# Optimization experiments

Measured on AMD Instinct MI355X. Metric: run time of the kernel, lower is better.

Reference implementation:

```python
import jax, jax.numpy as jnp
import numpy as np

N_NODES = 50000
N_EDGES = 800000


def setup_inputs() -> dict:
    key = jax.random.key(0)
    ks = jax.random.split(key, 9)
    d, h, hd = 128, 4, 32
    s = 1.0 / np.sqrt(d)
    return {
        "x": jax.random.normal(ks[0], (N_NODES, d), jnp.float32),
        "edge_index": jax.random.randint(ks[1], (2, N_EDGES), 0, N_NODES, jnp.int32),
        "W0": jax.random.normal(ks[2], (d, d), jnp.float32) * s,
        "att_l0": jax.random.normal(ks[3], (h, hd), jnp.float32) * s,
        "att_r0": jax.random.normal(ks[4], (h, hd), jnp.float32) * s,
        "b0": jnp.zeros((d,), jnp.float32),
        "W1": jax.random.normal(ks[5], (d, d), jnp.float32) * s,
        "att_l1": jax.random.normal(ks[6], (h, hd), jnp.float32) * s,
        "att_r1": jax.random.normal(ks[7], (h, hd), jnp.float32) * s,
        "b1": jnp.zeros((hd,), jnp.float32),
    }


def _gat_layer(x, src, dst, W, att_l, att_r, bias, concat):
    # x: [N, F_in]; W: [H*D, F_in] (torch Linear layout); att_*: [H, D]
    n = x.shape[0]
    h, d = att_l.shape
    hx = (x @ W.T).reshape(n, h, d)                     # [N,H,D]
    al = jnp.einsum('nhd,hd->nh', hx, att_l)            # [N,H]
    ar = jnp.einsum('nhd,hd->nh', hx, att_r)
    att = al[src] + ar[dst]                             # [E,H]
    att = jax.nn.leaky_relu(att, negative_slope=0.2)
    # segment softmax over destination nodes
    m = jax.ops.segment_max(att, dst, num_segments=n)   # [N,H]
    att = jnp.exp(att - m[dst])
    ssum = jax.ops.segment_sum(att, dst, num_segments=n)
    att = att / (ssum[dst] + 1e-9)                      # [E,H]
    msgs = att[:, :, None] * hx[src]                    # [E,H,D]
    out = jax.ops.segment_sum(msgs, dst, num_segments=n)  # [N,H,D]
    if concat:
        out = out.reshape(n, h * d)
    else:
        out = out.mean(axis=1)
    return out + bias


def reference(x, edge_index, W0, att_l0, att_r0, b0, W1, att_l1, att_r1, b1):
    src, dst = edge_index[0], edge_index[1]
    x = _gat_layer(x, src, dst, W0, att_l0, att_r0, b0, concat=True)
    x = jax.nn.relu(x)  # dropout is identity in eval mode
    x = _gat_layer(x, src, dst, W1, att_l1, att_r1, b1, concat=False)
    return x
```

## Files before the change

kernel.cpp:

```cpp
#include <hip/hip_runtime.h>
#include <hip/hip_bf16.h>

#define H 4
#define D 32
#define F 128
#define MAXDEG 64
#define PF 16
#define NBUCK 256
#define BUCKW 196
#define CAP   4096
#define NABLK 128

typedef __attribute__((ext_vector_type(8))) short bf16x8;
typedef __attribute__((ext_vector_type(4))) float f32x4;

__device__ __forceinline__ short f2bf(float v) {
    __hip_bfloat16 h = __float2bfloat16(v);
    return *reinterpret_cast<short*>(&h);
}
__device__ __forceinline__ float bf2f(short s) {
    __hip_bfloat16 h = *reinterpret_cast<__hip_bfloat16*>(&s);
    return __bfloat162float(h);
}

__device__ __forceinline__
void wconv_body(const float* __restrict__ W, short* __restrict__ Whi,
                short* __restrict__ Wlo) {
    for (int i = threadIdx.x * 4; i < F * F; i += 1024) {
        float4 v = *reinterpret_cast<const float4*>(W + i);
        float vv[4] = {v.x, v.y, v.z, v.w};
        short hs[4], ls[4];
#pragma unroll
        for (int j = 0; j < 4; ++j) {
            hs[j] = f2bf(vv[j]);
            ls[j] = f2bf(vv[j] - bf2f(hs[j]));
        }
        *reinterpret_cast<short4*>(Whi + i) = make_short4(hs[0], hs[1], hs[2], hs[3]);
        *reinterpret_cast<short4*>(Wlo + i) = make_short4(ls[0], ls[1], ls[2], ls[3]);
    }
}

__device__ __forceinline__
void bucketA_body(int abid, const int* __restrict__ ei, int E,
                  int* __restrict__ gcnt, unsigned int* __restrict__ buf) {
    __shared__ int lcnt[NBUCK];
    __shared__ int lpos[NBUCK];
    const int tid = threadIdx.x;
    lcnt[tid] = 0;
    __syncthreads();
    const int per = ((E / NABLK) + 3) & ~3;
    const int e0 = abid * per;
    const int e1 = min(e0 + per, E);
    for (int e = e0 + 4 * tid; e < e1; e += 1024) {
        int4 dv = *reinterpret_cast<const int4*>(ei + E + e);
        atomicAdd(&lcnt[dv.x / BUCKW], 1);
        atomicAdd(&lcnt[dv.y / BUCKW], 1);
        atomicAdd(&lcnt[dv.z / BUCKW], 1);
        atomicAdd(&lcnt[dv.w / BUCKW], 1);
    }
    __syncthreads();
    if (lcnt[tid] > 0)
        lpos[tid] = atomicAdd(&gcnt[tid], lcnt[tid]);
    __syncthreads();
    for (int e = e0 + 4 * tid; e < e1; e += 1024) {
        int4 sv = *reinterpret_cast<const int4*>(ei + e);
        int4 dv = *reinterpret_cast<const int4*>(ei + E + e);
        int ss[4] = {sv.x, sv.y, sv.z, sv.w};
        int dd[4] = {dv.x, dv.y, dv.z, dv.w};
#pragma unroll
        for (int j = 0; j < 4; ++j) {
            int b = dd[j] / BUCKW;
            int pos = atomicAdd(&lpos[b], 1);
            if (pos < CAP)
                buf[(size_t)b * CAP + pos] =
                    (unsigned)ss[j] | ((unsigned)(dd[j] - b * BUCKW) << 16);
        }
    }
}

__global__ __launch_bounds__(256)
void k_prep(const float* __restrict__ W0, short* __restrict__ W0hi,
            short* __restrict__ W0lo, const float* __restrict__ W1,
            short* __restrict__ W1hi, short* __restrict__ W1lo,
            const int* __restrict__ ei, int E,
            int* __restrict__ gcnt, unsigned int* __restrict__ buf) {
    if (blockIdx.x < NABLK)
        bucketA_body(blockIdx.x, ei, E, gcnt, buf);
    else if (blockIdx.x == NABLK)
        wconv_body(W0, W0hi, W0lo);
    else
        wconv_body(W1, W1hi, W1lo);
}

__device__ __forceinline__
void bucketB_body(int b, const unsigned int* __restrict__ buf,
                  const int* __restrict__ gcnt, int* __restrict__ deg,
                  unsigned short* __restrict__ ssrc2u, int N) {
    __shared__ int cnt[BUCKW];
    const int tid = threadIdx.x;
    if (tid < BUCKW) cnt[tid] = 0;
    __syncthreads();
    const int mm = min(gcnt[b], CAP);
    const int m4 = mm & ~3;
    for (int i = 4 * tid; i < m4; i += 1024) {
        uint4 r = *reinterpret_cast<const uint4*>(buf + (size_t)b * CAP + i);
        unsigned rr[4] = {r.x, r.y, r.z, r.w};
#pragma unroll
        for (int j = 0; j < 4; ++j) {
            int src  = rr[j] & 0xffff;
            int ldst = rr[j] >> 16;
            int slot = atomicAdd(&cnt[ldst], 1);
            if (slot < MAXDEG)
                ssrc2u[(size_t)(b * BUCKW + ldst) * MAXDEG + slot] = (unsigned short)src;
        }
    }
    for (int i = m4 + tid; i < mm; i += 256) {
        unsigned rec = buf[(size_t)b * CAP + i];
        int src  = rec & 0xffff;
        int ldst = rec >> 16;
        int slot = atomicAdd(&cnt[ldst], 1);
        if (slot < MAXDEG)
            ssrc2u[(size_t)(b * BUCKW + ldst) * MAXDEG + slot] = (unsigned short)src;
    }
    __syncthreads();
    if (tid < BUCKW) {
        int node = b * BUCKW + tid;
        if (node < N) deg[node] = cnt[tid];
    }
}

template<bool AFP32>
__device__ __forceinline__
void gemm_core(int bid, int nblocks, const void* __restrict__ Xv,
               const short* __restrict__ Xlo_, const short* __restrict__ Whi,
               const short* __restrict__ Wlo, const float* __restrict__ attl,
               const float* __restrict__ attr, __hip_bfloat16* __restrict__ HXB,
               float* __restrict__ AL, float* __restrict__ AR, int ntiles) {
    const int wave = threadIdx.x >> 6;
    const int lane = threadIdx.x & 63;
    const int m    = lane & 15;
    const int q    = lane >> 4;
    const int q8   = q * 8;

    bf16x8 Bhi[2][4], Blo[2][4];
#pragma unroll
    for (int j = 0; j < 2; ++j) {
        const int fout = wave * 32 + j * 16 + m;
#pragma unroll
        for (int kc = 0; kc < 4; ++kc) {
            Bhi[j][kc] = *reinterpret_cast<const bf16x8*>(Whi + (size_t)fout * F + kc * 32 + q8);
            Blo[j][kc] = *reinterpret_cast<const bf16x8*>(Wlo + (size_t)fout * F + kc * 32 + q8);
        }
    }
    const float alw0  = attl[wave * 32 + m];
    const float alw16 = attl[wave * 32 + 16 + m];
    const float arw0  = attr[wave * 32 + m];
    const float arw16 = attr[wave * 32 + 16 + m];

    for (int tile = bid; tile < ntiles; tile += nblocks) {
        const int node0 = tile * 16;
        bf16x8 Ahi[4], Alo[4];
        if constexpr (AFP32) {
            const float* xp = reinterpret_cast<const float*>(Xv) + (size_t)(node0 + m) * F + q8;
#pragma unroll
            for (int kc = 0; kc < 4; ++kc) {
                float4 x0 = *reinterpret_cast<const float4*>(xp + kc * 32);
                float4 x1 = *reinterpret_cast<const float4*>(xp + kc * 32 + 4);
                float xv[8] = {x0.x, x0.y, x0.z, x0.w, x1.x, x1.y, x1.z, x1.w};
#pragma unroll
                for (int t = 0; t < 8; ++t) {
                    short h = f2bf(xv[t]);
                    Ahi[kc][t] = h;
                    Alo[kc][t] = f2bf(xv[t] - bf2f(h));
                }
            }
        } else {
            const short* xh = reinterpret_cast<const short*>(Xv) + (size_t)(node0 + m) * F + q8;
            const short* xl = Xlo_ + (size_t)(node0 + m) * F + q8;
#pragma unroll
            for (int kc = 0; kc < 4; ++kc) {
                Ahi[kc] = *reinterpret_cast<const bf16x8*>(xh + kc * 32);
                Alo[kc] = *reinterpret_cast<const bf16x8*>(xl + kc * 32);
            }
        }
        f32x4 acc0 = {0.f, 0.f, 0.f, 0.f};
        f32x4 acc1 = {0.f, 0.f, 0.f, 0.f};
#pragma unroll
        for (int kc = 0; kc < 4; ++kc) {
            acc0 = __builtin_amdgcn_mfma_f32_16x16x32_bf16(Ahi[kc], Bhi[0][kc], acc0, 0, 0, 0);
            acc1 = __builtin_amdgcn_mfma_f32_16x16x32_bf16(Ahi[kc], Bhi[1][kc], acc1, 0, 0, 0);
            acc0 = __builtin_amdgcn_mfma_f32_16x16x32_bf16(Ahi[kc], Blo[0][kc], acc0, 0, 0, 0);
            acc1 = __builtin_amdgcn_mfma_f32_16x16x32_bf16(Ahi[kc], Blo[1][kc], acc1, 0, 0, 0);
            acc0 = __builtin_amdgcn_mfma_f32_16x16x32_bf16(Alo[kc], Bhi[0][kc], acc0, 0, 0, 0);
            acc1 = __builtin_amdgcn_mfma_f32_16x16x32_bf16(Alo[kc], Bhi[1][kc], acc1, 0, 0, 0);
        }
        const int row0 = node0 + q * 4;
        const int col0 = wave * 32 + m;
#pragma unroll
        for (int r = 0; r < 4; ++r) {
            HXB[(size_t)(row0 + r) * F + col0]      = __float2bfloat16(acc0[r]);
            HXB[(size_t)(row0 + r) * F + col0 + 16] = __float2bfloat16(acc1[r]);
            float pal = acc0[r] * alw0 + acc1[r] * alw16;
            float par = acc0[r] * arw0 + acc1[r] * arw16;
#pragma unroll
            for (int o = 1; o < 16; o <<= 1) {
                pal += __shfl_xor(pal, o);
                par += __shfl_xor(par, o);
            }
            if (m == 0) {
                AL[(size_t)(row0 + r) * H + wave] = pal;
                AR[(size_t)(row0 + r) * H + wave] = par;
            }
        }
    }
}

__global__ __launch_bounds__(256)
void k_g0(const unsigned int* __restrict__ buf, const int* __restrict__ gcnt,
          int* __restrict__ deg, unsigned short* __restrict__ ssrc2u, int N,
          const float* __restrict__ X, const short* __restrict__ W0hi,
          const short* __restrict__ W0lo, const float* __restrict__ attl0,
          const float* __restrict__ attr0, __hip_bfloat16* __restrict__ HXB,
          float* __restrict__ AL, float* __restrict__ AR, int ntiles) {
    if (blockIdx.x < NBUCK)
        bucketB_body(blockIdx.x, buf, gcnt, deg, ssrc2u, N);
    else
        gemm_core<true>(blockIdx.x - NBUCK, gridDim.x - NBUCK, X, nullptr,
                        W0hi, W0lo, attl0, attr0, HXB, AL, AR, ntiles);
}

__global__ __launch_bounds__(256)
void k_gemm1(const short* __restrict__ X1hi, const short* __restrict__ X1lo,
             const short* __restrict__ W1hi, const short* __restrict__ W1lo,
             const float* __restrict__ attl, const float* __restrict__ attr,
             __hip_bfloat16* __restrict__ HXB, float* __restrict__ AL,
             float* __restrict__ AR, int ntiles) {
    gemm_core<false>(blockIdx.x, gridDim.x, X1hi, X1lo, W1hi, W1lo,
                     attl, attr, HXB, AL, AR, ntiles);
}

__device__ __forceinline__
int stage_node(int g, int t, int n, const unsigned short* __restrict__ ssrc2u,
               const int* __restrict__ deg, const float* __restrict__ AL,
               const float4 ar4, int (*sidx)[MAXDEG], float (*sw)[MAXDEG][H]) {
    const int cnt  = min(deg[n], MAXDEG);
    const int rcnt = (cnt + PF - 1) & ~(PF - 1);
    if (t < rcnt) {
        if (t < cnt) {
            int s = ssrc2u[n * MAXDEG + t];
            sidx[g][t] = s;
            float4 al4 = *reinterpret_cast<const float4*>(AL + (size_t)s * H);
            float a0 = al4.x + ar4.x; a0 = a0 > 0.f ? a0 : 0.2f * a0;
            float a1 = al4.y + ar4.y; a1 = a1 > 0.f ? a1 : 0.2f * a1;
            float a2 = al4.z + ar4.z; a2 = a2 > 0.f ? a2 : 0.2f * a2;
            float a3 = al4.w + ar4.w; a3 = a3 > 0.f ? a3 : 0.2f * a3;
            sw[g][t][0] = __expf(a0);
            sw[g][t][1] = __expf(a1);
            sw[g][t][2] = __expf(a2);
            sw[g][t][3] = __expf(a3);
        } else {
            sidx[g][t] = 0;
            sw[g][t][0] = 0.f; sw[g][t][1] = 0.f; sw[g][t][2] = 0.f; sw[g][t][3] = 0.f;
        }
    }
    __builtin_amdgcn_wave_barrier();
    return rcnt;
}

__device__ __forceinline__
void gather_node(int g, int t, int h, int rcnt, const __hip_bfloat16* __restrict__ HXB,
                 const int (*sidx)[MAXDEG], const float (*sw)[MAXDEG][H],
                 float& accx, float& accy, float& wsum) {
    for (int base = 0; base < rcnt; base += PF) {
        __hip_bfloat162 v[PF];
#pragma unroll
        for (int j = 0; j < PF; ++j) {
            int s = sidx[g][base + j];
            v[j] = *reinterpret_cast<const __hip_bfloat162*>(HXB + (size_t)s * F + 2 * t);
        }
#pragma unroll
        for (int j = 0; j < PF; ++j) {
            float w = sw[g][base + j][h];
            float2 f = __bfloat1622float2(v[j]);
            accx += w * f.x;
            accy += w * f.y;
            wsum += w;
        }
    }
}

__global__ __launch_bounds__(256)
void k_aggr0(const unsigned short* __restrict__ ssrc2u, const int* __restrict__ deg,
             const float* __restrict__ AL, const float* __restrict__ AR,
             const __hip_bfloat16* __restrict__ HXB, const float* __restrict__ bias,
             short* __restrict__ X1hi, short* __restrict__ X1lo, int N) {
    __shared__ int   sidx[4][MAXDEG];
    __shared__ float sw[4][MAXDEG][H];
    const int g = threadIdx.x >> 6;
    const int t = threadIdx.x & 63;
    const int n = blockIdx.x * 4 + g;
    if (n >= N) return;
    const int h = t >> 4;
    const float4 ar4 = *reinterpret_cast<const float4*>(AR + (size_t)n * H);
    int rcnt = stage_node(g, t, n, ssrc2u, deg, AL, ar4, sidx, sw);
    float accx = 0.f, accy = 0.f, wsum = 0.f;
    gather_node(g, t, h, rcnt, HXB, sidx, sw, accx, accy, wsum);
    float inv = 1.f / (wsum + 1e-9f);
    float ox = fmaxf(accx * inv + bias[2 * t], 0.f);
    float oy = fmaxf(accy * inv + bias[2 * t + 1], 0.f);
    short h0 = f2bf(ox), h1 = f2bf(oy);
    short l0 = f2bf(ox - bf2f(h0)), l1 = f2bf(oy - bf2f(h1));
    unsigned hw = (unsigned)(unsigned short)h0 | ((unsigned)(unsigned short)h1 << 16);
    unsigned lw = (unsigned)(unsigned short)l0 | ((unsigned)(unsigned short)l1 << 16);
    *reinterpret_cast<unsigned*>(X1hi + (size_t)n * F + 2 * t) = hw;
    *reinterpret_cast<unsigned*>(X1lo + (size_t)n * F + 2 * t) = lw;
}

__global__ __launch_bounds__(256)
void k_aggr1(const unsigned short* __restrict__ ssrc2u, const int* __restrict__ deg,
             const float* __restrict__ AL, const float* __restrict__ AR,
             const __hip_bfloat16* __restrict__ HXB, const float* __restrict__ bias,
             float* __restrict__ out, int N) {
    __shared__ int   sidx[4][MAXDEG];
    __shared__ float sw[4][MAXDEG][H];
    const int g = threadIdx.x >> 6;
    const int t = threadIdx.x & 63;
    const int n = blockIdx.x * 4 + g;
    if (n >= N) return;
    const int h = t >> 4;
    const float4 ar4 = *reinterpret_cast<const float4*>(AR + (size_t)n * H);
    int rcnt = stage_node(g, t, n, ssrc2u, deg, AL, ar4, sidx, sw);
    float accx = 0.f, accy = 0.f, wsum = 0.f;
    gather_node(g, t, h, rcnt, HXB, sidx, sw, accx, accy, wsum);
    float inv = 1.f / (wsum + 1e-9f);
    float vx = accx * inv, vy = accy * inv;
    vx += __shfl_xor(vx, 16); vx += __shfl_xor(vx, 32);
    vy += __shfl_xor(vy, 16); vy += __shfl_xor(vy, 32);
    if (t < 16) {
        float2 o;
        o.x = 0.25f * vx + bias[2 * t];
        o.y = 0.25f * vy + bias[2 * t + 1];
        *reinterpret_cast<float2*>(out + (size_t)n * D + 2 * t) = o;
    }
}

extern "C" void kernel_launch(void* const* d_in, const int* in_sizes, int n_in,
                              void* d_out, int out_size, void* d_ws, size_t ws_size,
                              hipStream_t stream) {
    const float* x     = (const float*)d_in[0];
    const int*   ei    = (const int*)d_in[1];
    const float* W0    = (const float*)d_in[2];
    const float* attl0 = (const float*)d_in[3];
    const float* attr0 = (const float*)d_in[4];
    const float* b0    = (const float*)d_in[5];
    const float* W1    = (const float*)d_in[6];
    const float* attl1 = (const float*)d_in[7];
    const float* attr1 = (const float*)d_in[8];
    const float* b1    = (const float*)d_in[9];

    const int N = in_sizes[0] / F;
    const int E = in_sizes[1] / 2;
    const int ntiles = N / 16;

    char* p = (char*)d_ws;
    __hip_bfloat16* HXB = (__hip_bfloat16*)p;   p += (size_t)N * F * 2;
    short* X1hi = (short*)p;                    p += (size_t)N * F * 2;
    short* X1lo = (short*)p;                    p += (size_t)N * F * 2;
    short* W0hi = (short*)p;                    p += (size_t)F * F * 2;
    short* W0lo = (short*)p;                    p += (size_t)F * F * 2;
    short* W1hi = (short*)p;                    p += (size_t)F * F * 2;
    short* W1lo = (short*)p;                    p += (size_t)F * F * 2;
    float* AL   = (float*)p;                    p += (size_t)N * H * 4;
    float* AR   = (float*)p;                    p += (size_t)N * H * 4;
    unsigned short* ssrc2u = (unsigned short*)p; p += (size_t)N * MAXDEG * 2;
    int* deg = (int*)p;                         p += (size_t)N * 4;
    unsigned int* buf = (unsigned int*)p;       p += (size_t)NBUCK * CAP * 4;
    int* gcnt = (int*)p;

    hipMemsetAsync(gcnt, 0, NBUCK * sizeof(int), stream);

    k_prep<<<NABLK + 2, 256, 0, stream>>>(W0, W0hi, W0lo, W1, W1hi, W1lo,
                                          ei, E, gcnt, buf);

    k_g0<<<NBUCK + ntiles, 256, 0, stream>>>(buf, gcnt, deg, ssrc2u, N,
                                             x, W0hi, W0lo, attl0, attr0,
                                             HXB, AL, AR, ntiles);

    k_aggr0<<<(N + 3) / 4, 256, 0, stream>>>(ssrc2u, deg, AL, AR, HXB, b0,
                                             X1hi, X1lo, N);

    k_gemm1<<<ntiles, 256, 0, stream>>>(X1hi, X1lo, W1hi, W1lo, attl1, attr1,
                                        HXB, AL, AR, ntiles);

    k_aggr1<<<(N + 3) / 4, 256, 0, stream>>>(ssrc2u, deg, AL, AR, HXB, b1,
                                             (float*)d_out, N);
}
```

Before: 244.0 us.

## Fuse all GAT stages into one persistent cooperative kernel with grid syncs

Replaces the five launches (prep, bucketB+gemm0, aggr0, gemm1, aggr1) with one cooperative persistent kernel. Stages are separated by grid.sync, the layer-0 GEMM takes tiles from a dynamic atomic counter, and the W0 hi/lo split is done in registers instead of a separate conversion pass. The aim is to remove launch gaps and overlap bucketing with the first GEMM. In exchange, grid-wide barriers are costly, the grid is capped by occupancy, and the persistent loops may balance work worse than many small blocks did.

```diff
diff --git a/kernel.cpp b/kernel.cpp
--- a/kernel.cpp
+++ b/kernel.cpp
@@ -1,5 +1,8 @@
 #include <hip/hip_runtime.h>
 #include <hip/hip_bf16.h>
+#include <hip/hip_cooperative_groups.h>
+
+namespace cg = cooperative_groups;
 
 #define H 4
 #define D 32
@@ -9,7 +12,7 @@
 #define NBUCK 256
 #define BUCKW 196
 #define CAP   4096
-#define NABLK 128
+#define NABLK 256
 
 typedef __attribute__((ext_vector_type(8))) short bf16x8;
 typedef __attribute__((ext_vector_type(4))) float f32x4;
@@ -78,20 +81,6 @@
     }
 }
 
-__global__ __launch_bounds__(256)
-void k_prep(const float* __restrict__ W0, short* __restrict__ W0hi,
-            short* __restrict__ W0lo, const float* __restrict__ W1,
-            short* __restrict__ W1hi, short* __restrict__ W1lo,
-            const int* __restrict__ ei, int E,
-            int* __restrict__ gcnt, unsigned int* __restrict__ buf) {
-    if (blockIdx.x < NABLK)
-        bucketA_body(blockIdx.x, ei, E, gcnt, buf);
-    else if (blockIdx.x == NABLK)
-        wconv_body(W0, W0hi, W0lo);
-    else
-        wconv_body(W1, W1hi, W1lo);
-}
-
 __device__ __forceinline__
 void bucketB_body(int b, const unsigned int* __restrict__ buf,
                   const int* __restrict__ gcnt, int* __restrict__ deg,
@@ -129,20 +118,31 @@
     }
 }
 
-template<bool AFP32>
-__device__ __forceinline__
-void gemm_core(int bid, int nblocks, const void* __restrict__ Xv,
-               const short* __restrict__ Xlo_, const short* __restrict__ Whi,
-               const short* __restrict__ Wlo, const float* __restrict__ attl,
-               const float* __restrict__ attr, __hip_bfloat16* __restrict__ HXB,
-               float* __restrict__ AL, float* __restrict__ AR, int ntiles) {
-    const int wave = threadIdx.x >> 6;
-    const int lane = threadIdx.x & 63;
-    const int m    = lane & 15;
-    const int q    = lane >> 4;
-    const int q8   = q * 8;
-
-    bf16x8 Bhi[2][4], Blo[2][4];
+__device__ __forceinline__
+void bsetup_fp32(const float* __restrict__ W, int wave, int m, int q8,
+                 bf16x8 Bhi[2][4], bf16x8 Blo[2][4]) {
+#pragma unroll
+    for (int j = 0; j < 2; ++j) {
+        const int fout = wave * 32 + j * 16 + m;
+#pragma unroll
+        for (int kc = 0; kc < 4; ++kc) {
+            const float* wp = W + (size_t)fout * F + kc * 32 + q8;
+            float4 w0 = *reinterpret_cast<const float4*>(wp);
+            float4 w1 = *reinterpret_cast<const float4*>(wp + 4);
+            float wv[8] = {w0.x, w0.y, w0.z, w0.w, w1.x, w1.y, w1.z, w1.w};
+#pragma unroll
+            for (int t2 = 0; t2 < 8; ++t2) {
+                short hh = f2bf(wv[t2]);
+                Bhi[j][kc][t2] = hh;
+                Blo[j][kc][t2] = f2bf(wv[t2] - bf2f(hh));
+            }
+        }
+    }
+}
+
+__device__ __forceinline__
+void bsetup_pre(const short* __restrict__ Whi, const short* __restrict__ Wlo,
+                int wave, int m, int q8, bf16x8 Bhi[2][4], bf16x8 Blo[2][4]) {
 #pragma unroll
     for (int j = 0; j < 2; ++j) {
         const int fout = wave * 32 + j * 16 + m;
@@ -152,97 +152,86 @@
             Blo[j][kc] = *reinterpret_cast<const bf16x8*>(Wlo + (size_t)fout * F + kc * 32 + q8);
         }
     }
-    const float alw0  = attl[wave * 32 + m];
-    const float alw16 = attl[wave * 32 + 16 + m];
-    const float arw0  = attr[wave * 32 + m];
-    const float arw16 = attr[wave * 32 + 16 + m];
-
-    for (int tile = bid; tile < ntiles; tile += nblocks) {
-        const int node0 = tile * 16;
-        bf16x8 Ahi[4], Alo[4];
-        if constexpr (AFP32) {
-            const float* xp = reinterpret_cast<const float*>(Xv) + (size_t)(node0 + m) * F + q8;
-#pragma unroll
-            for (int kc = 0; kc < 4; ++kc) {
-                float4 x0 = *reinterpret_cast<const float4*>(xp + kc * 32);
-                float4 x1 = *reinterpret_cast<const float4*>(xp + kc * 32 + 4);
-                float xv[8] = {x0.x, x0.y, x0.z, x0.w, x1.x, x1.y, x1.z, x1.w};
-#pragma unroll
-                for (int t = 0; t < 8; ++t) {
-                    short h = f2bf(xv[t]);
-                    Ahi[kc][t] = h;
-                    Alo[kc][t] = f2bf(xv[t] - bf2f(h));
-                }
+}
+
+template<bool AFP32>
+__device__ __forceinline__
+void gemm_tile(int tile, const void* __restrict__ Xv, const short* __restrict__ Xlo_,
+               const bf16x8 Bhi[2][4], const bf16x8 Blo[2][4],
+               float alw0, float alw16, float arw0, float arw16,
+               __hip_bfloat16* __restrict__ HXB, float* __restrict__ AL,
+               float* __restrict__ AR, int wave, int m, int q) {
+    const int q8 = q * 8;
+    const int node0 = tile * 16;
+    bf16x8 Ahi[4], Alo[4];
+    if constexpr (AFP32) {
+        const float* xp = reinterpret_cast<const float*>(Xv) + (size_t)(node0 + m) * F + q8;
+#pragma unroll
+        for (int kc = 0; kc < 4; ++kc) {
+            float4 x0 = *reinterpret_cast<const float4*>(xp + kc * 32);
+            float4 x1 = *reinterpret_cast<const float4*>(xp + kc * 32 + 4);
+            float xv[8] = {x0.x, x0.y, x0.z, x0.w, x1.x, x1.y, x1.z, x1.w};
+#pragma unroll
+            for (int t2 = 0; t2 < 8; ++t2) {
+                short hh = f2bf(xv[t2]);
+                Ahi[kc][t2] = hh;
+                Alo[kc][t2] = f2bf(xv[t2] - bf2f(hh));
             }
-        } else {
-            const short* xh = reinterpret_cast<const short*>(Xv) + (size_t)(node0 + m) * F + q8;
-            const short* xl = Xlo_ + (size_t)(node0 + m) * F + q8;
-#pragma unroll
-            for (int kc = 0; kc < 4; ++kc) {
-                Ahi[kc] = *reinterpret_cast<const bf16x8*>(xh + kc * 32);
-                Alo[kc] = *reinterpret_cast<const bf16x8*>(xl + kc * 32);
-            }
-        }
-        f32x4 acc0 = {0.f, 0.f, 0.f, 0.f};
-        f32x4 acc1 = {0.f, 0.f, 0.f, 0.f};
+        }
+    } else {
+        const short* xh = reinterpret_cast<const short*>(Xv) + (size_t)(node0 + m) * F + q8;
+        const short* xl = Xlo_ + (size_t)(node0 + m) * F + q8;
 #pragma unroll
         for (int kc = 0; kc < 4; ++kc) {
-            acc0 = __builtin_amdgcn_mfma_f32_16x16x32_bf16(Ahi[kc], Bhi[0][kc], acc0, 0, 0, 0);
-            acc1 = __builtin_amdgcn_mfma_f32_16x16x32_bf16(Ahi[kc], Bhi[1][kc], acc1, 0, 0, 0);
-            acc0 = __builtin_amdgcn_mfma_f32_16x16x32_bf16(Ahi[kc], Blo[0][kc], acc0, 0, 0, 0);
-            acc1 = __builtin_amdgcn_mfma_f32_16x16x32_bf16(Ahi[kc], Blo[1][kc], acc1, 0, 0, 0);
-            acc0 = __builtin_amdgcn_mfma_f32_16x16x32_bf16(Alo[kc], Bhi[0][kc], acc0, 0, 0, 0);
-            acc1 = __builtin_amdgcn_mfma_f32_16x16x32_bf16(Alo[kc], Bhi[1][kc], acc1, 0, 0, 0);
-        }
-        const int row0 = node0 + q * 4;
-        const int col0 = wave * 32 + m;
-#pragma unroll
-        for (int r = 0; r < 4; ++r) {
-            HXB[(size_t)(row0 + r) * F + col0]      = __float2bfloat16(acc0[r]);
-            HXB[(size_t)(row0 + r) * F + col0 + 16] = __float2bfloat16(acc1[r]);
-            float pal = acc0[r] * alw0 + acc1[r] * alw16;
-            float par = acc0[r] * arw0 + acc1[r] * arw16;
-#pragma unroll
-            for (int o = 1; o < 16; o <<= 1) {
-                pal += __shfl_xor(pal, o);
-                par += __shfl_xor(par, o);
-            }
-            if (m == 0) {
-                AL[(size_t)(row0 + r) * H + wave] = pal;
-                AR[(size_t)(row0 + r) * H + wave] = par;
-            }
-        }
-    }
-}
-
-__global__ __launch_bounds__(256)
-void k_g0(const unsigned int* __restrict__ buf, const int* __restrict__ gcnt,
-          int* __restrict__ deg, unsigned short* __restrict__ ssrc2u, int N,
-          const float* __restrict__ X, const short* __restrict__ W0hi,
-          const short* __restrict__ W0lo, const float* __restrict__ attl0,
-          const float* __restrict__ attr0, __hip_bfloat16* __restrict__ HXB,
-          float* __restrict__ AL, float* __restrict__ AR, int ntiles) {
-    if (blockIdx.x < NBUCK)
-        bucketB_body(blockIdx.x, buf, gcnt, deg, ssrc2u, N);
-    else
-        gemm_core<true>(blockIdx.x - NBUCK, gridDim.x - NBUCK, X, nullptr,
-                        W0hi, W0lo, attl0, attr0, HXB, AL, AR, ntiles);
-}
-
-__global__ __launch_bounds__(256)
-void k_gemm1(const short* __restrict__ X1hi, const short* __restrict__ X1lo,
-             const short* __restrict__ W1hi, const short* __restrict__ W1lo,
-             const float* __restrict__ attl, const float* __restrict__ attr,
-             __hip_bfloat16* __restrict__ HXB, float* __restrict__ AL,
-             float* __restrict__ AR, int ntiles) {
-    gemm_core<false>(blockIdx.x, gridDim.x, X1hi, X1lo, W1hi, W1lo,
-                     attl, attr, HXB, AL, AR, ntiles);
-}
-
-__device__ __forceinline__
-int stage_node(int g, int t, int n, const unsigned short* __restrict__ ssrc2u,
-               const int* __restrict__ deg, const float* __restrict__ AL,
-               const float4 ar4, int (*sidx)[MAXDEG], float (*sw)[MAXDEG][H]) {
+            Ahi[kc] = *reinterpret_cast<const bf16x8*>(xh + kc * 32);
+            Alo[kc] = *reinterpret_cast<const bf16x8*>(xl + kc * 32);
+        }
+    }
+    f32x4 acc0 = {0.f, 0.f, 0.f, 0.f};
+    f32x4 acc1 = {0.f, 0.f, 0.f, 0.f};
+#pragma unroll
+    for (int kc = 0; kc < 4; ++kc) {
+        acc0 = __builtin_amdgcn_mfma_f32_16x16x32_bf16(Ahi[kc], Bhi[0][kc], acc0, 0, 0, 0);
+        acc1 = __builtin_amdgcn_mfma_f32_16x16x32_bf16(Ahi[kc], Bhi[1][kc], acc1, 0, 0, 0);
+        acc0 = __builtin_amdgcn_mfma_f32_16x16x32_bf16(Ahi[kc], Blo[0][kc], acc0, 0, 0, 0);
+        acc1 = __builtin_amdgcn_mfma_f32_16x16x32_bf16(Ahi[kc], Blo[1][kc], acc1, 0, 0, 0);
+        acc0 = __builtin_amdgcn_mfma_f32_16x16x32_bf16(Alo[kc], Bhi[0][kc], acc0, 0, 0, 0);
+        acc1 = __builtin_amdgcn_mfma_f32_16x16x32_bf16(Alo[kc], Bhi[1][kc], acc1, 0, 0, 0);
+    }
+    const int row0 = node0 + q * 4;
+    const int col0 = wave * 32 + m;
+#pragma unroll
+    for (int r = 0; r < 4; ++r) {
+        HXB[(size_t)(row0 + r) * F + col0]      = __float2bfloat16(acc0[r]);
+        HXB[(size_t)(row0 + r) * F + col0 + 16] = __float2bfloat16(acc1[r]);
+        float pal = acc0[r] * alw0 + acc1[r] * alw16;
+        float par = acc0[r] * arw0 + acc1[r] * arw16;
+#pragma unroll
+        for (int o = 1; o < 16; o <<= 1) {
+            pal += __shfl_xor(pal, o);
+            par += __shfl_xor(par, o);
+        }
+        if (m == 0) {
+            AL[(size_t)(row0 + r) * H + wave] = pal;
+            AR[(size_t)(row0 + r) * H + wave] = par;
+        }
+    }
+}
+
+__device__ __forceinline__
+void aggr_body(int nb, bool layer1,
+               const unsigned short* __restrict__ ssrc2u, const int* __restrict__ deg,
+               const float* __restrict__ AL, const float* __restrict__ AR,
+               const __hip_bfloat16* __restrict__ HXB, const float* __restrict__ bias,
+               short* __restrict__ X1hi, short* __restrict__ X1lo,
+               float* __restrict__ out, int N,
+               int (*sidx)[MAXDEG], float (*sw)[MAXDEG][H]) {
+    const int g = threadIdx.x >> 6;
+    const int t = threadIdx.x & 63;
+    const int n = nb * 4 + g;
+    if (n >= N) return;
+    const int h = t >> 4;
+    const float4 ar4 = *reinterpret_cast<const float4*>(AR + (size_t)n * H);
     const int cnt  = min(deg[n], MAXDEG);
     const int rcnt = (cnt + PF - 1) & ~(PF - 1);
     if (t < rcnt) {
@@ -264,13 +253,7 @@
         }
     }
     __builtin_amdgcn_wave_barrier();
-    return rcnt;
-}
-
-__device__ __forceinline__
-void gather_node(int g, int t, int h, int rcnt, const __hip_bfloat16* __restrict__ HXB,
-                 const int (*sidx)[MAXDEG], const float (*sw)[MAXDEG][H],
-                 float& accx, float& accy, float& wsum) {
+    float accx = 0.f, accy = 0.f, wsum = 0.f;
     for (int base = 0; base < rcnt; base += PF) {
         __hip_bfloat162 v[PF];
 #pragma unroll
@@ -287,61 +270,105 @@
             wsum += w;
         }
     }
-}
-
-__global__ __launch_bounds__(256)
-void k_aggr0(const unsigned short* __restrict__ ssrc2u, const int* __restrict__ deg,
-             const float* __restrict__ AL, const float* __restrict__ AR,
-             const __hip_bfloat16* __restrict__ HXB, const float* __restrict__ bias,
-             short* __restrict__ X1hi, short* __restrict__ X1lo, int N) {
+    float inv = 1.f / (wsum + 1e-9f);
+    if (!layer1) {
+        float ox = fmaxf(accx * inv + bias[2 * t], 0.f);
+        float oy = fmaxf(accy * inv + bias[2 * t + 1], 0.f);
+        short h0 = f2bf(ox), h1 = f2bf(oy);
+        short l0 = f2bf(ox - bf2f(h0)), l1 = f2bf(oy - bf2f(h1));
+        unsigned hw = (unsigned)(unsigned short)h0 | ((unsigned)(unsigned short)h1 << 16);
+        unsigned lw = (unsigned)(unsigned short)l0 | ((unsigned)(unsigned short)l1 << 16);
+        *reinterpret_cast<unsigned*>(X1hi + (size_t)n * F + 2 * t) = hw;
+        *reinterpret_cast<unsigned*>(X1lo + (size_t)n * F + 2 * t) = lw;
+    } else {
+        float vx = accx * inv, vy = accy * inv;
+        vx += __shfl_xor(vx, 16); vx += __shfl_xor(vx, 32);
+        vy += __shfl_xor(vy, 16); vy += __shfl_xor(vy, 32);
+        if (t < 16) {
+            float2 o;
+            o.x = 0.25f * vx + bias[2 * t];
+            o.y = 0.25f * vy + bias[2 * t + 1];
+            *reinterpret_cast<float2*>(out + (size_t)n * D + 2 * t) = o;
+        }
+    }
+}
+
+__global__ __launch_bounds__(256, 4)
+void k_fused(const float* __restrict__ X, const float* __restrict__ W0,
+             const float* __restrict__ attl0, const float* __restrict__ attr0,
+             const float* __restrict__ b0, const float* __restrict__ W1,
+             const float* __restrict__ attl1, const float* __restrict__ attr1,
+             const float* __restrict__ b1, const int* __restrict__ ei,
+             int E, int N, int ntiles,
+             __hip_bfloat16* __restrict__ HXB, short* __restrict__ X1hi,
+             short* __restrict__ X1lo, short* __restrict__ W1hi,
+             short* __restrict__ W1lo, float* __restrict__ AL,
+             float* __restrict__ AR, unsigned short* __restrict__ ssrc2u,
+             int* __restrict__ deg, unsigned int* __restrict__ buf,
+             int* __restrict__ gcnt, int* __restrict__ tileCtr,
+             float* __restrict__ out) {
+    cg::grid_group grid = cg::this_grid();
+    const int bid  = blockIdx.x;
+    const int tid  = threadIdx.x;
+    const int nblk = gridDim.x;
+    const int wave = tid >> 6;
+    const int lane = tid & 63;
+    const int m    = lane & 15;
+    const int q    = lane >> 4;
+    const int q8   = q * 8;
+
+    __shared__ int   stile;
     __shared__ int   sidx[4][MAXDEG];
     __shared__ float sw[4][MAXDEG][H];
-    const int g = threadIdx.x >> 6;
-    const int t = threadIdx.x & 63;
-    const int n = blockIdx.x * 4 + g;
-    if (n >= N) return;
-    const int h = t >> 4;
-    const float4 ar4 = *reinterpret_cast<const float4*>(AR + (size_t)n * H);
-    int rcnt = stage_node(g, t, n, ssrc2u, deg, AL, ar4, sidx, sw);
-    float accx = 0.f, accy = 0.f, wsum = 0.f;
-    gather_node(g, t, h, rcnt, HXB, sidx, sw, accx, accy, wsum);
-    float inv = 1.f / (wsum + 1e-9f);
-    float ox = fmaxf(accx * inv + bias[2 * t], 0.f);
-    float oy = fmaxf(accy * inv + bias[2 * t + 1], 0.f);
-    short h0 = f2bf(ox), h1 = f2bf(oy);
-    short l0 = f2bf(ox - bf2f(h0)), l1 = f2bf(oy - bf2f(h1));
-    unsigned hw = (unsigned)(unsigned short)h0 | ((unsigned)(unsigned short)h1 << 16);
-    unsigned lw = (unsigned)(unsigned short)l0 | ((unsigned)(unsigned short)l1 << 16);
-    *reinterpret_cast<unsigned*>(X1hi + (size_t)n * F + 2 * t) = hw;
-    *reinterpret_cast<unsigned*>(X1lo + (size_t)n * F + 2 * t) = lw;
-}
-
-__global__ __launch_bounds__(256)
-void k_aggr1(const unsigned short* __restrict__ ssrc2u, const int* __restrict__ deg,
-             const float* __restrict__ AL, const float* __restrict__ AR,
-             const __hip_bfloat16* __restrict__ HXB, const float* __restrict__ bias,
-             float* __restrict__ out, int N) {
-    __shared__ int   sidx[4][MAXDEG];
-    __shared__ float sw[4][MAXDEG][H];
-    const int g = threadIdx.x >> 6;
-    const int t = threadIdx.x & 63;
-    const int n = blockIdx.x * 4 + g;
-    if (n >= N) return;
-    const int h = t >> 4;
-    const float4 ar4 = *reinterpret_cast<const float4*>(AR + (size_t)n * H);
-    int rcnt = stage_node(g, t, n, ssrc2u, deg, AL, ar4, sidx, sw);
-    float accx = 0.f, accy = 0.f, wsum = 0.f;
-    gather_node(g, t, h, rcnt, HXB, sidx, sw, accx, accy, wsum);
-    float inv = 1.f / (wsum + 1e-9f);
-    float vx = accx * inv, vy = accy * inv;
-    vx += __shfl_xor(vx, 16); vx += __shfl_xor(vx, 32);
-    vy += __shfl_xor(vy, 16); vy += __shfl_xor(vy, 32);
-    if (t < 16) {
-        float2 o;
-        o.x = 0.25f * vx + bias[2 * t];
-        o.y = 0.25f * vy + bias[2 * t + 1];
-        *reinterpret_cast<float2*>(out + (size_t)n * D + 2 * t) = o;
-    }
+
+    if (bid < NABLK) {
+        bucketA_body(bid, ei, E, gcnt, buf);
+        if (bid == 0) wconv_body(W1, W1hi, W1lo);
+    }
+    {
+        bf16x8 Bhi[2][4], Blo[2][4];
+        bsetup_fp32(W0, wave, m, q8, Bhi, Blo);
+        const float alw0  = attl0[wave * 32 + m];
+        const float alw16 = attl0[wave * 32 + 16 + m];
+        const float arw0  = attr0[wave * 32 + m];
+        const float arw16 = attr0[wave * 32 + 16 + m];
+        while (true) {
+            __syncthreads();
+            if (tid == 0) stile = atomicAdd(tileCtr, 1);
+            __syncthreads();
+            int t = stile;
+            if (t >= ntiles) break;
+            gemm_tile<true>(t, X, nullptr, Bhi, Blo, alw0, alw16, arw0, arw16,
+                            HXB, AL, AR, wave, m, q);
+        }
+    }
+    grid.sync();
+
+    for (int b = bid; b < NBUCK; b += nblk)
+        bucketB_body(b, buf, gcnt, deg, ssrc2u, N);
+    grid.sync();
+
+    for (int nb = bid; nb < (N + 3) / 4; nb += nblk)
+        aggr_body(nb, false, ssrc2u, deg, AL, AR, HXB, b0, X1hi, X1lo,
+                  nullptr, N, sidx, sw);
+    grid.sync();
+
+    {
+        bf16x8 Bhi[2][4], Blo[2][4];
+        bsetup_pre(W1hi, W1lo, wave, m, q8, Bhi, Blo);
+        const float alw0  = attl1[wave * 32 + m];
+        const float alw16 = attl1[wave * 32 + 16 + m];
+        const float arw0  = attr1[wave * 32 + m];
+        const float arw16 = attr1[wave * 32 + 16 + m];
+        for (int t = bid; t < ntiles; t += nblk)
+            gemm_tile<false>(t, X1hi, X1lo, Bhi, Blo, alw0, alw16, arw0, arw16,
+                             HXB, AL, AR, wave, m, q);
+    }
+    grid.sync();
+
+    for (int nb = bid; nb < (N + 3) / 4; nb += nblk)
+        aggr_body(nb, true, ssrc2u, deg, AL, AR, HXB, b1, nullptr, nullptr,
+                  out, N, sidx, sw);
 }
 
 extern "C" void kernel_launch(void* const* d_in, const int* in_sizes, int n_in,
@@ -358,16 +385,14 @@
     const float* attr1 = (const float*)d_in[8];
     const float* b1    = (const float*)d_in[9];
 
-    const int N = in_sizes[0] / F;
-    const int E = in_sizes[1] / 2;
-    const int ntiles = N / 16;
+    int N = in_sizes[0] / F;
+    int E = in_sizes[1] / 2;
+    int ntiles = N / 16;
 
     char* p = (char*)d_ws;
     __hip_bfloat16* HXB = (__hip_bfloat16*)p;   p += (size_t)N * F * 2;
     short* X1hi = (short*)p;                    p += (size_t)N * F * 2;
     short* X1lo = (short*)p;                    p += (size_t)N * F * 2;
-    short* W0hi = (short*)p;                    p += (size_t)F * F * 2;
-    short* W0lo = (short*)p;                    p += (size_t)F * F * 2;
     short* W1hi = (short*)p;                    p += (size_t)F * F * 2;
     short* W1lo = (short*)p;                    p += (size_t)F * F * 2;
     float* AL   = (float*)p;                    p += (size_t)N * H * 4;
@@ -375,23 +400,28 @@
     unsigned short* ssrc2u = (unsigned short*)p; p += (size_t)N * MAXDEG * 2;
     int* deg = (int*)p;                         p += (size_t)N * 4;
     unsigned int* buf = (unsigned int*)p;       p += (size_t)NBUCK * CAP * 4;
-    int* gcnt = (int*)p;
-
-    hipMemsetAsync(gcnt, 0, NBUCK * sizeof(int), stream);
-
-    k_prep<<<NABLK + 2, 256, 0, stream>>>(W0, W0hi, W0lo, W1, W1hi, W1lo,
-                                          ei, E, gcnt, buf);
-
-    k_g0<<<NBUCK + ntiles, 256, 0, stream>>>(buf, gcnt, deg, ssrc2u, N,
-                                             x, W0hi, W0lo, attl0, attr0,
-                                             HXB, AL, AR, ntiles);
-
-    k_aggr0<<<(N + 3) / 4, 256, 0, stream>>>(ssrc2u, deg, AL, AR, HXB, b0,
-                                             X1hi, X1lo, N);
-
-    k_gemm1<<<ntiles, 256, 0, stream>>>(X1hi, X1lo, W1hi, W1lo, attl1, attr1,
-                                        HXB, AL, AR, ntiles);
-
-    k_aggr1<<<(N + 3) / 4, 256, 0, stream>>>(ssrc2u, deg, AL, AR, HXB, b1,
-                                             (float*)d_out, N);
-}
+    int* gcnt = (int*)p;                        p += (size_t)NBUCK * 4;
+    int* tileCtr = (int*)p;
+
+    hipMemsetAsync(gcnt, 0, (NBUCK + 1) * sizeof(int), stream);
+
+    int maxB = 4;
+    (void)hipOccupancyMaxActiveBlocksPerMultiprocessor(&maxB, (const void*)k_fused,
+                                                       256, 0);
+    if (maxB < 1) maxB = 1;
+    if (maxB > 8) maxB = 8;
+    int nblk = 256 * maxB;
+    if (nblk < NABLK) nblk = NABLK;
+
+    float* outp = (float*)d_out;
+    void* args[] = {
+        (void*)&x, (void*)&W0, (void*)&attl0, (void*)&attr0, (void*)&b0,
+        (void*)&W1, (void*)&attl1, (void*)&attr1, (void*)&b1,
+        (void*)&ei, (void*)&E, (void*)&N, (void*)&ntiles,
+        (void*)&HXB, (void*)&X1hi, (void*)&X1lo, (void*)&W1hi, (void*)&W1lo,
+        (void*)&AL, (void*)&AR, (void*)&ssrc2u, (void*)&deg,
+        (void*)&buf, (void*)&gcnt, (void*)&tileCtr, (void*)&outp
+    };
+    hipLaunchCooperativeKernel((const void*)k_fused, dim3(nblk), dim3(256),
+                               args, 0, stream);
+}
```

New measurement: 541.6 us. 122% more time.

## Restructure launch schedule: fuse layer-0 GEMM with bucketing, two tiles per block

Applied to the files above, without the earlier changes.

Weight conversion and the zeroing of the bucket counters move into a small init kernel, which replaces the memset. The layer-0 GEMM is then co-scheduled with the first bucketing pass instead of the second. Each GEMM block now handles two tiles with their loads issued up front, so there are fewer blocks and memory latency can overlap. The second bucketing pass builds each bucket's adjacency in shared memory and writes it out with coalesced 16-byte stores instead of scattered 2-byte stores. The costs are larger shared-memory use per bucket block, which can lower occupancy, and a fixed GB constant that ties the pairing to this node count.

```diff
diff --git a/kernel.cpp b/kernel.cpp
--- a/kernel.cpp
+++ b/kernel.cpp
@@ -10,6 +10,7 @@
 #define BUCKW 196
 #define CAP   4096
 #define NABLK 128
+#define GB    1563
 
 typedef __attribute__((ext_vector_type(8))) short bf16x8;
 typedef __attribute__((ext_vector_type(4))) float f32x4;
@@ -23,10 +24,20 @@
     return __bfloat162float(h);
 }
 
-__device__ __forceinline__
-void wconv_body(const float* __restrict__ W, short* __restrict__ Whi,
-                short* __restrict__ Wlo) {
-    for (int i = threadIdx.x * 4; i < F * F; i += 1024) {
+__global__ __launch_bounds__(256)
+void k_init(const float* __restrict__ W0, short* __restrict__ W0hi,
+            short* __restrict__ W0lo, const float* __restrict__ W1,
+            short* __restrict__ W1hi, short* __restrict__ W1lo,
+            int* __restrict__ gcnt) {
+    const int bid = blockIdx.x;
+    const int tid = threadIdx.x;
+    if (bid == 0) gcnt[tid] = 0;
+    const float* W  = (bid < 4) ? W0 : W1;
+    short* Whi = (bid < 4) ? W0hi : W1hi;
+    short* Wlo = (bid < 4) ? W0lo : W1lo;
+    const int part = bid & 3;
+    const int base = part * (F * F / 4);
+    for (int i = base + tid * 4; i < base + F * F / 4; i += 1024) {
         float4 v = *reinterpret_cast<const float4*>(W + i);
         float vv[4] = {v.x, v.y, v.z, v.w};
         short hs[4], ls[4];
@@ -78,25 +89,175 @@
     }
 }
 
-__global__ __launch_bounds__(256)
-void k_prep(const float* __restrict__ W0, short* __restrict__ W0hi,
-            short* __restrict__ W0lo, const float* __restrict__ W1,
-            short* __restrict__ W1hi, short* __restrict__ W1lo,
-            const int* __restrict__ ei, int E,
-            int* __restrict__ gcnt, unsigned int* __restrict__ buf) {
-    if (blockIdx.x < NABLK)
-        bucketA_body(blockIdx.x, ei, E, gcnt, buf);
-    else if (blockIdx.x == NABLK)
-        wconv_body(W0, W0hi, W0lo);
+__device__ __forceinline__
+void bsetup_pre(const short* __restrict__ Whi, const short* __restrict__ Wlo,
+                int wave, int m, int q8, bf16x8 Bhi[2][4], bf16x8 Blo[2][4]) {
+#pragma unroll
+    for (int j = 0; j < 2; ++j) {
+        const int fout = wave * 32 + j * 16 + m;
+#pragma unroll
+        for (int kc = 0; kc < 4; ++kc) {
+            Bhi[j][kc] = *reinterpret_cast<const bf16x8*>(Whi + (size_t)fout * F + kc * 32 + q8);
+            Blo[j][kc] = *reinterpret_cast<const bf16x8*>(Wlo + (size_t)fout * F + kc * 32 + q8);
+        }
+    }
+}
+
+__device__ __forceinline__
+void loadA_f32(const float* __restrict__ X, int node0, int m, int q8, float4 r[8]) {
+    const float* xp = X + (size_t)(node0 + m) * F + q8;
+#pragma unroll
+    for (int kc = 0; kc < 4; ++kc) {
+        r[2 * kc]     = *reinterpret_cast<const float4*>(xp + kc * 32);
+        r[2 * kc + 1] = *reinterpret_cast<const float4*>(xp + kc * 32 + 4);
+    }
+}
+
+__device__ __forceinline__
+void splitA(const float4 r[8], bf16x8 Ahi[4], bf16x8 Alo[4]) {
+#pragma unroll
+    for (int kc = 0; kc < 4; ++kc) {
+        float xv[8] = {r[2 * kc].x, r[2 * kc].y, r[2 * kc].z, r[2 * kc].w,
+                       r[2 * kc + 1].x, r[2 * kc + 1].y, r[2 * kc + 1].z, r[2 * kc + 1].w};
+#pragma unroll
+        for (int t2 = 0; t2 < 8; ++t2) {
+            short hh = f2bf(xv[t2]);
+            Ahi[kc][t2] = hh;
+            Alo[kc][t2] = f2bf(xv[t2] - bf2f(hh));
+        }
+    }
+}
+
+__device__ __forceinline__
+void loadA_bf(const short* __restrict__ Xhi, const short* __restrict__ Xlo,
+              int node0, int m, int q8, bf16x8 Ahi[4], bf16x8 Alo[4]) {
+    const short* xh = Xhi + (size_t)(node0 + m) * F + q8;
+    const short* xl = Xlo + (size_t)(node0 + m) * F + q8;
+#pragma unroll
+    for (int kc = 0; kc < 4; ++kc) {
+        Ahi[kc] = *reinterpret_cast<const bf16x8*>(xh + kc * 32);
+        Alo[kc] = *reinterpret_cast<const bf16x8*>(xl + kc * 32);
+    }
+}
+
+__device__ __forceinline__
+void mfma_epi(int tile, const bf16x8 Ahi[4], const bf16x8 Alo[4],
+              const bf16x8 Bhi[2][4], const bf16x8 Blo[2][4],
+              float alw0, float alw16, float arw0, float arw16,
+              __hip_bfloat16* __restrict__ HXB, float* __restrict__ AL,
+              float* __restrict__ AR, int wave, int m, int q) {
+    const int node0 = tile * 16;
+    f32x4 acc0 = {0.f, 0.f, 0.f, 0.f};
+    f32x4 acc1 = {0.f, 0.f, 0.f, 0.f};
+#pragma unroll
+    for (int kc = 0; kc < 4; ++kc) {
+        acc0 = __builtin_amdgcn_mfma_f32_16x16x32_bf16(Ahi[kc], Bhi[0][kc], acc0, 0, 0, 0);
+        acc1 = __builtin_amdgcn_mfma_f32_16x16x32_bf16(Ahi[kc], Bhi[1][kc], acc1, 0, 0, 0);
+        acc0 = __builtin_amdgcn_mfma_f32_16x16x32_bf16(Ahi[kc], Blo[0][kc], acc0, 0, 0, 0);
+        acc1 = __builtin_amdgcn_mfma_f32_16x16x32_bf16(Ahi[kc], Blo[1][kc], acc1, 0, 0, 0);
+        acc0 = __builtin_amdgcn_mfma_f32_16x16x32_bf16(Alo[kc], Bhi[0][kc], acc0, 0, 0, 0);
+        acc1 = __builtin_amdgcn_mfma_f32_16x16x32_bf16(Alo[kc], Bhi[1][kc], acc1, 0, 0, 0);
+    }
+    const int row0 = node0 + q * 4;
+    const int col0 = wave * 32 + m;
+#pragma unroll
+    for (int r = 0; r < 4; ++r) {
+        HXB[(size_t)(row0 + r) * F + col0]      = __float2bfloat16(acc0[r]);
+        HXB[(size_t)(row0 + r) * F + col0 + 16] = __float2bfloat16(acc1[r]);
+        float pal = acc0[r] * alw0 + acc1[r] * alw16;
+        float par = acc0[r] * arw0 + acc1[r] * arw16;
+#pragma unroll
+        for (int o = 1; o < 16; o <<= 1) {
+            pal += __shfl_xor(pal, o);
+            par += __shfl_xor(par, o);
+        }
+        if (m == 0) {
+            AL[(size_t)(row0 + r) * H + wave] = pal;
+            AR[(size_t)(row0 + r) * H + wave] = par;
+        }
+    }
+}
+
+__device__ __forceinline__
+void gemm_pair_f32(int bid, const float* __restrict__ X,
+                   const short* __restrict__ Whi, const short* __restrict__ Wlo,
+                   const float* __restrict__ attl, const float* __restrict__ attr,
+                   __hip_bfloat16* __restrict__ HXB, float* __restrict__ AL,
+                   float* __restrict__ AR, int ntiles) {
+    const int wave = threadIdx.x >> 6;
+    const int lane = threadIdx.x & 63;
+    const int m    = lane & 15;
+    const int q    = lane >> 4;
+    const int q8   = q * 8;
+    bf16x8 Bhi[2][4], Blo[2][4];
+    bsetup_pre(Whi, Wlo, wave, m, q8, Bhi, Blo);
+    const float alw0  = attl[wave * 32 + m];
+    const float alw16 = attl[wave * 32 + 16 + m];
+    const float arw0  = attr[wave * 32 + m];
+    const float arw16 = attr[wave * 32 + 16 + m];
+
+    const int t0 = bid, t1 = bid + GB;
+    const bool has1 = t1 < ntiles;
+    float4 r0[8], r1[8];
+    loadA_f32(X, t0 * 16, m, q8, r0);
+    if (has1) loadA_f32(X, t1 * 16, m, q8, r1);
+    bf16x8 Ahi[4], Alo[4];
+    splitA(r0, Ahi, Alo);
+    mfma_epi(t0, Ahi, Alo, Bhi, Blo, alw0, alw16, arw0, arw16, HXB, AL, AR, wave, m, q);
+    if (has1) {
+        splitA(r1, Ahi, Alo);
+        mfma_epi(t1, Ahi, Alo, Bhi, Blo, alw0, alw16, arw0, arw16, HXB, AL, AR, wave, m, q);
+    }
+}
+
+__device__ __forceinline__
+void gemm_pair_bf(int bid, const short* __restrict__ Xhi, const short* __restrict__ Xlo,
+                  const short* __restrict__ Whi, const short* __restrict__ Wlo,
+                  const float* __restrict__ attl, const float* __restrict__ attr,
+                  __hip_bfloat16* __restrict__ HXB, float* __restrict__ AL,
+                  float* __restrict__ AR, int ntiles) {
+    const int wave = threadIdx.x >> 6;
+    const int lane = threadIdx.x & 63;
+    const int m    = lane & 15;
+    const int q    = lane >> 4;
+    const int q8   = q * 8;
+    bf16x8 Bhi[2][4], Blo[2][4];
+    bsetup_pre(Whi, Wlo, wave, m, q8, Bhi, Blo);
+    const float alw0  = attl[wave * 32 + m];
+    const float alw16 = attl[wave * 32 + 16 + m];
+    const float arw0  = attr[wave * 32 + m];
+    const float arw16 = attr[wave * 32 + 16 + m];
+
+    const int t0 = bid, t1 = bid + GB;
+    const bool has1 = t1 < ntiles;
+    bf16x8 A0h[4], A0l[4], A1h[4], A1l[4];
+    loadA_bf(Xhi, Xlo, t0 * 16, m, q8, A0h, A0l);
+    if (has1) loadA_bf(Xhi, Xlo, t1 * 16, m, q8, A1h, A1l);
+    mfma_epi(t0, A0h, A0l, Bhi, Blo, alw0, alw16, arw0, arw16, HXB, AL, AR, wave, m, q);
+    if (has1)
+        mfma_epi(t1, A1h, A1l, Bhi, Blo, alw0, alw16, arw0, arw16, HXB, AL, AR, wave, m, q);
+}
+
+__global__ __launch_bounds__(256)
+void k_pre(const float* __restrict__ X, const short* __restrict__ W0hi,
+           const short* __restrict__ W0lo, const float* __restrict__ attl0,
+           const float* __restrict__ attr0, __hip_bfloat16* __restrict__ HXB,
+           float* __restrict__ AL, float* __restrict__ AR, int ntiles,
+           const int* __restrict__ ei, int E,
+           int* __restrict__ gcnt, unsigned int* __restrict__ buf) {
+    const int bid = blockIdx.x;
+    if (bid < GB)
+        gemm_pair_f32(bid, X, W0hi, W0lo, attl0, attr0, HXB, AL, AR, ntiles);
     else
-        wconv_body(W1, W1hi, W1lo);
-}
-
-__device__ __forceinline__
-void bucketB_body(int b, const unsigned int* __restrict__ buf,
-                  const int* __restrict__ gcnt, int* __restrict__ deg,
-                  unsigned short* __restrict__ ssrc2u, int N) {
+        bucketA_body(bid - GB, ei, E, gcnt, buf);
+}
+
+__global__ __launch_bounds__(256)
+void k_bucket(const unsigned int* __restrict__ buf, const int* __restrict__ gcnt,
+              int* __restrict__ deg, unsigned short* __restrict__ ssrc2u, int N) {
     __shared__ int cnt[BUCKW];
+    __shared__ unsigned short slots[BUCKW * MAXDEG];
+    const int b = blockIdx.x;
     const int tid = threadIdx.x;
     if (tid < BUCKW) cnt[tid] = 0;
     __syncthreads();
@@ -111,7 +272,7 @@
             int ldst = rr[j] >> 16;
             int slot = atomicAdd(&cnt[ldst], 1);
             if (slot < MAXDEG)
-                ssrc2u[(size_t)(b * BUCKW + ldst) * MAXDEG + slot] = (unsigned short)src;
+                slots[ldst * MAXDEG + slot] = (unsigned short)src;
         }
     }
     for (int i = m4 + tid; i < mm; i += 256) {
@@ -120,123 +281,17 @@
         int ldst = rec >> 16;
         int slot = atomicAdd(&cnt[ldst], 1);
         if (slot < MAXDEG)
-            ssrc2u[(size_t)(b * BUCKW + ldst) * MAXDEG + slot] = (unsigned short)src;
+            slots[ldst * MAXDEG + slot] = (unsigned short)src;
     }
     __syncthreads();
+    uint4* dst = reinterpret_cast<uint4*>(ssrc2u + (size_t)b * BUCKW * MAXDEG);
+    const uint4* s4 = reinterpret_cast<const uint4*>(slots);
+    for (int i = tid; i < BUCKW * MAXDEG / 8; i += 256)
+        dst[i] = s4[i];
     if (tid < BUCKW) {
         int node = b * BUCKW + tid;
         if (node < N) deg[node] = cnt[tid];
     }
-}
-
-template<bool AFP32>
-__device__ __forceinline__
-void gemm_core(int bid, int nblocks, const void* __restrict__ Xv,
-               const short* __restrict__ Xlo_, const short* __restrict__ Whi,
-               const short* __restrict__ Wlo, const float* __restrict__ attl,
-               const float* __restrict__ attr, __hip_bfloat16* __restrict__ HXB,
-               float* __restrict__ AL, float* __restrict__ AR, int ntiles) {
-    const int wave = threadIdx.x >> 6;
-    const int lane = threadIdx.x & 63;
-    const int m    = lane & 15;
-    const int q    = lane >> 4;
-    const int q8   = q * 8;
-
-    bf16x8 Bhi[2][4], Blo[2][4];
-#pragma unroll
-    for (int j = 0; j < 2; ++j) {
-        const int fout = wave * 32 + j * 16 + m;
-#pragma unroll
-        for (int kc = 0; kc < 4; ++kc) {
-            Bhi[j][kc] = *reinterpret_cast<const bf16x8*>(Whi + (size_t)fout * F + kc * 32 + q8);
-            Blo[j][kc] = *reinterpret_cast<const bf16x8*>(Wlo + (size_t)fout * F + kc * 32 + q8);
-        }
-    }
-    const float alw0  = attl[wave * 32 + m];
-    const float alw16 = attl[wave * 32 + 16 + m];
-    const float arw0  = attr[wave * 32 + m];
-    const float arw16 = attr[wave * 32 + 16 + m];
-
-    for (int tile = bid; tile < ntiles; tile += nblocks) {
-        const int node0 = tile * 16;
-        bf16x8 Ahi[4], Alo[4];
-        if constexpr (AFP32) {
-            const float* xp = reinterpret_cast<const float*>(Xv) + (size_t)(node0 + m) * F + q8;
-#pragma unroll
-            for (int kc = 0; kc < 4; ++kc) {
-                float4 x0 = *reinterpret_cast<const float4*>(xp + kc * 32);
-                float4 x1 = *reinterpret_cast<const float4*>(xp + kc * 32 + 4);
-                float xv[8] = {x0.x, x0.y, x0.z, x0.w, x1.x, x1.y, x1.z, x1.w};
-#pragma unroll
-                for (int t = 0; t < 8; ++t) {
-                    short h = f2bf(xv[t]);
-                    Ahi[kc][t] = h;
-                    Alo[kc][t] = f2bf(xv[t] - bf2f(h));
-                }
-            }
-        } else {
-            const short* xh = reinterpret_cast<const short*>(Xv) + (size_t)(node0 + m) * F + q8;
-            const short* xl = Xlo_ + (size_t)(node0 + m) * F + q8;
-#pragma unroll
-            for (int kc = 0; kc < 4; ++kc) {
-                Ahi[kc] = *reinterpret_cast<const bf16x8*>(xh + kc * 32);
-                Alo[kc] = *reinterpret_cast<const bf16x8*>(xl + kc * 32);
-            }
-        }
-        f32x4 acc0 = {0.f, 0.f, 0.f, 0.f};
-        f32x4 acc1 = {0.f, 0.f, 0.f, 0.f};
-#pragma unroll
-        for (int kc = 0; kc < 4; ++kc) {
-            acc0 = __builtin_amdgcn_mfma_f32_16x16x32_bf16(Ahi[kc], Bhi[0][kc], acc0, 0, 0, 0);
-            acc1 = __builtin_amdgcn_mfma_f32_16x16x32_bf16(Ahi[kc], Bhi[1][kc], acc1, 0, 0, 0);
-            acc0 = __builtin_amdgcn_mfma_f32_16x16x32_bf16(Ahi[kc], Blo[0][kc], acc0, 0, 0, 0);
-            acc1 = __builtin_amdgcn_mfma_f32_16x16x32_bf16(Ahi[kc], Blo[1][kc], acc1, 0, 0, 0);
-            acc0 = __builtin_amdgcn_mfma_f32_16x16x32_bf16(Alo[kc], Bhi[0][kc], acc0, 0, 0, 0);
-            acc1 = __builtin_amdgcn_mfma_f32_16x16x32_bf16(Alo[kc], Bhi[1][kc], acc1, 0, 0, 0);
-        }
-        const int row0 = node0 + q * 4;
-        const int col0 = wave * 32 + m;
-#pragma unroll
-        for (int r = 0; r < 4; ++r) {
-            HXB[(size_t)(row0 + r) * F + col0]      = __float2bfloat16(acc0[r]);
-            HXB[(size_t)(row0 + r) * F + col0 + 16] = __float2bfloat16(acc1[r]);
-            float pal = acc0[r] * alw0 + acc1[r] * alw16;
-            float par = acc0[r] * arw0 + acc1[r] * arw16;
-#pragma unroll
-            for (int o = 1; o < 16; o <<= 1) {
-                pal += __shfl_xor(pal, o);
-                par += __shfl_xor(par, o);
-            }
-            if (m == 0) {
-                AL[(size_t)(row0 + r) * H + wave] = pal;
-                AR[(size_t)(row0 + r) * H + wave] = par;
-            }
-        }
-    }
-}
-
-__global__ __launch_bounds__(256)
-void k_g0(const unsigned int* __restrict__ buf, const int* __restrict__ gcnt,
-          int* __restrict__ deg, unsigned short* __restrict__ ssrc2u, int N,
-          const float* __restrict__ X, const short* __restrict__ W0hi,
-          const short* __restrict__ W0lo, const float* __restrict__ attl0,
-          const float* __restrict__ attr0, __hip_bfloat16* __restrict__ HXB,
-          float* __restrict__ AL, float* __restrict__ AR, int ntiles) {
-    if (blockIdx.x < NBUCK)
-        bucketB_body(blockIdx.x, buf, gcnt, deg, ssrc2u, N);
-    else
-        gemm_core<true>(blockIdx.x - NBUCK, gridDim.x - NBUCK, X, nullptr,
-                        W0hi, W0lo, attl0, attr0, HXB, AL, AR, ntiles);
-}
-
-__global__ __launch_bounds__(256)
-void k_gemm1(const short* __restrict__ X1hi, const short* __restrict__ X1lo,
-             const short* __restrict__ W1hi, const short* __restrict__ W1lo,
-             const float* __restrict__ attl, const float* __restrict__ attr,
-             __hip_bfloat16* __restrict__ HXB, float* __restrict__ AL,
-             float* __restrict__ AR, int ntiles) {
-    gemm_core<false>(blockIdx.x, gridDim.x, X1hi, X1lo, W1hi, W1lo,
-                     attl, attr, HXB, AL, AR, ntiles);
 }
 
 __device__ __forceinline__
@@ -247,7 +302,7 @@
     const int rcnt = (cnt + PF - 1) & ~(PF - 1);
     if (t < rcnt) {
         if (t < cnt) {
-            int s = ssrc2u[n * MAXDEG + t];
+            int s = ssrc2u[(size_t)n * MAXDEG + t];
             sidx[g][t] = s;
             float4 al4 = *reinterpret_cast<const float4*>(AL + (size_t)s * H);
             float a0 = al4.x + ar4.x; a0 = a0 > 0.f ? a0 : 0.2f * a0;
@@ -317,6 +372,16 @@
 }
 
 __global__ __launch_bounds__(256)
+void k_gemm1(const short* __restrict__ X1hi, const short* __restrict__ X1lo,
+             const short* __restrict__ W1hi, const short* __restrict__ W1lo,
+             const float* __restrict__ attl, const float* __restrict__ attr,
+             __hip_bfloat16* __restrict__ HXB, float* __restrict__ AL,
+             float* __restrict__ AR, int ntiles) {
+    gemm_pair_bf(blockIdx.x, X1hi, X1lo, W1hi, W1lo, attl, attr,
+                 HXB, AL, AR, ntiles);
+}
+
+__global__ __launch_bounds__(256)
 void k_aggr1(const unsigned short* __restrict__ ssrc2u, const int* __restrict__ deg,
              const float* __restrict__ AL, const float* __restrict__ AR,
              const __hip_bfloat16* __restrict__ HXB, const float* __restrict__ bias,
@@ -372,25 +437,24 @@
     short* W1lo = (short*)p;                    p += (size_t)F * F * 2;
     float* AL   = (float*)p;                    p += (size_t)N * H * 4;
     float* AR   = (float*)p;                    p += (size_t)N * H * 4;
-    unsigned short* ssrc2u = (unsigned short*)p; p += (size_t)N * MAXDEG * 2;
+    unsigned short* ssrc2u = (unsigned short*)p;
+    p += (size_t)NBUCK * BUCKW * MAXDEG * 2;
     int* deg = (int*)p;                         p += (size_t)N * 4;
     unsigned int* buf = (unsigned int*)p;       p += (size_t)NBUCK * CAP * 4;
     int* gcnt = (int*)p;
 
-    hipMemsetAsync(gcnt, 0, NBUCK * sizeof(int), stream);
-
-    k_prep<<<NABLK + 2, 256, 0, stream>>>(W0, W0hi, W0lo, W1, W1hi, W1lo,
-                                          ei, E, gcnt, buf);
-
-    k_g0<<<NBUCK + ntiles, 256, 0, stream>>>(buf, gcnt, deg, ssrc2u, N,
-                                             x, W0hi, W0lo, attl0, attr0,
-                                             HXB, AL, AR, ntiles);
+    k_init<<<8, 256, 0, stream>>>(W0, W0hi, W0lo, W1, W1hi, W1lo, gcnt);
+
+    k_pre<<<GB + NABLK, 256, 0, stream>>>(x, W0hi, W0lo, attl0, attr0,
+                                          HXB, AL, AR, ntiles, ei, E, gcnt, buf);
+
+    k_bucket<<<NBUCK, 256, 0, stream>>>(buf, gcnt, deg, ssrc2u, N);
 
     k_aggr0<<<(N + 3) / 4, 256, 0, stream>>>(ssrc2u, deg, AL, AR, HXB, b0,
                                              X1hi, X1lo, N);
 
-    k_gemm1<<<ntiles, 256, 0, stream>>>(X1hi, X1lo, W1hi, W1lo, attl1, attr1,
-                                        HXB, AL, AR, ntiles);
+    k_gemm1<<<GB, 256, 0, stream>>>(X1hi, X1lo, W1hi, W1lo, attl1, attr1,
+                                    HXB, AL, AR, ntiles);
 
     k_aggr1<<<(N + 3) / 4, 256, 0, stream>>>(ssrc2u, deg, AL, AR, HXB, b1,
                                              (float*)d_out, N);
```

Result: faster. 222.9 us (-8.6%).
